# Optimization experiments

Hardware: AMD Instinct MI355X
Metric: run time of the kernel (lower is better)

Reference implementation:

```python
import jax, jax.numpy as jnp
import numpy as np

B, C, N, K = 2, 64, 16384, 16
C_OUT = 64


def setup_inputs() -> dict:
    key = jax.random.key(0)
    k1, k2, k3, k4 = jax.random.split(key, 4)
    x = jax.random.normal(k1, (B, C, N), dtype=jnp.float32)
    edge_index = jax.random.randint(k2, (2, B, N, K), 0, N, dtype=jnp.int64)
    # 1x1 Conv2d params: weight [C_out, 3C], bias [C_out]
    W = jax.random.normal(k3, (C_OUT, 3 * C), dtype=jnp.float32) * (1.0 / np.sqrt(3 * C))
    b = jax.random.normal(k4, (C_OUT,), dtype=jnp.float32) * 0.01
    return {"x": x, "edge_index": edge_index, "W": W, "b": b}


def _gather_nodes(x, idx):
    # x: [B, C, N], idx: [B, N, K] -> [B, C, N, K]
    return jax.vmap(lambda xb, ib: xb[:, ib])(x, idx)


def reference(x, edge_index, W, b):
    # x: [B, C, N]; edge_index: [2, B, N, K]
    x_i = _gather_nodes(x, edge_index[1])          # center features  [B,C,N,K]
    x_j = _gather_nodes(x, edge_index[0])          # neighbor features [B,C,N,K]
    edge_features = x_j - x_i                      # [B,C,N,K]
    global_feature = jnp.mean(x, axis=2, keepdims=True)  # [B,C,1] global mean over nodes
    global_rep = jnp.broadcast_to(global_feature[..., None], x_i.shape)  # [B,C,N,K]
    combined = jnp.concatenate([x_i, edge_features, global_rep], axis=1)  # [B,3C,N,K]
    # BasicConv: 1x1 conv + ReLU (norm=None)
    out = jnp.einsum("bcnk,oc->bonk", combined, W) + b[None, :, None, None]
    out = jax.nn.relu(out)
    return jnp.max(out, axis=-1, keepdims=True)    # [B,C_out,N,1]
```

## Files before the change

### kernel.cpp

```cpp
#include <hip/hip_runtime.h>


#define NNODES 16384
#define NCH 64

typedef _Float16 half8 __attribute__((ext_vector_type(8)));
typedef float f32x2 __attribute__((ext_vector_type(2)));
typedef float f32x4 __attribute__((ext_vector_type(4)));

__global__ __launch_bounds__(64) void prep_kernel(const float* __restrict__ W,
                                                  float2* __restrict__ ABg,
                                                  float* __restrict__ g_slots) {
  int o = blockIdx.x;
  int t = threadIdx.x;
  if (o == 0) {
#pragma unroll
    for (int i = 0; i < 16; ++i) g_slots[t + i * 64] = 0.0f;
  }
  float w1 = W[o * 192 + t];
  float w2 = W[o * 192 + 64 + t];
  ABg[t * 64 + o] = make_float2(w1 - w2, w2);
}

__global__ __launch_bounds__(256) void uv_kernel(const float* __restrict__ x,
                                                 const float2* __restrict__ ABg,
                                                 _Float16* __restrict__ u,
                                                 _Float16* __restrict__ v,
                                                 float* __restrict__ g_slots) {
  __shared__ float2 ABs[64 * 64];
  __shared__ float xs[64][64];
  __shared__ float csumS[64];
  int t = threadIdx.x;
  int lane = t & 63;
  int wv = __builtin_amdgcn_readfirstlane(t >> 6);
  int blk = blockIdx.x;
  int b = blk >> 8;
  int mb = (blk & 255) * 64;

  {
    const float4* src = (const float4*)ABg;
    float4* dst = (float4*)ABs;
#pragma unroll
    for (int j = 0; j < 8; ++j) dst[t + j * 256] = src[t + j * 256];
  }
  {
    const float* xb = x + (size_t)b * (NCH * NNODES) + mb;
    int off = t & 15;
#pragma unroll
    for (int j = 0; j < 4; ++j) {
      int c = (t >> 4) + j * 16;
      f32x4 q = __builtin_nontemporal_load(
          (const f32x4*)(xb + (size_t)c * NNODES + off * 4));
      *(f32x4*)&xs[c][off * 4] = q;
      float s = (q.x + q.y) + (q.z + q.w);
      s += __shfl_xor(s, 1, 16);
      s += __shfl_xor(s, 2, 16);
      s += __shfl_xor(s, 4, 16);
      s += __shfl_xor(s, 8, 16);
      if (off == 0) csumS[c] = s;
    }
  }
  __syncthreads();
  if (t < 64) atomicAdd(&g_slots[((blk & 7) << 7) + b * 64 + t], csumS[t]);

  int m0 = wv * 16;
  f32x2 aU[8], aV[8];
#pragma unroll
  for (int i = 0; i < 8; ++i) {
    aU[i] = (f32x2){0.f, 0.f};
    aV[i] = (f32x2){0.f, 0.f};
  }
#pragma unroll 8
  for (int c = 0; c < 64; ++c) {
    float2 ab = ABs[c * 64 + lane];
    f32x2 a2 = {ab.x, ab.x};
    f32x2 b2 = {ab.y, ab.y};
    const f32x4* xr = (const f32x4*)&xs[c][m0];
    f32x4 q0 = xr[0];
    f32x4 q1 = xr[1];
    f32x4 q2 = xr[2];
    f32x4 q3 = xr[3];
    f32x2 p0 = {q0.x, q0.y}, p1 = {q0.z, q0.w};
    f32x2 p2 = {q1.x, q1.y}, p3 = {q1.z, q1.w};
    f32x2 p4 = {q2.x, q2.y}, p5 = {q2.z, q2.w};
    f32x2 p6 = {q3.x, q3.y}, p7 = {q3.z, q3.w};
    aU[0] = __builtin_elementwise_fma(a2, p0, aU[0]);
    aU[1] = __builtin_elementwise_fma(a2, p1, aU[1]);
    aU[2] = __builtin_elementwise_fma(a2, p2, aU[2]);
    aU[3] = __builtin_elementwise_fma(a2, p3, aU[3]);
    aU[4] = __builtin_elementwise_fma(a2, p4, aU[4]);
    aU[5] = __builtin_elementwise_fma(a2, p5, aU[5]);
    aU[6] = __builtin_elementwise_fma(a2, p6, aU[6]);
    aU[7] = __builtin_elementwise_fma(a2, p7, aU[7]);
    aV[0] = __builtin_elementwise_fma(b2, p0, aV[0]);
    aV[1] = __builtin_elementwise_fma(b2, p1, aV[1]);
    aV[2] = __builtin_elementwise_fma(b2, p2, aV[2]);
    aV[3] = __builtin_elementwise_fma(b2, p3, aV[3]);
    aV[4] = __builtin_elementwise_fma(b2, p4, aV[4]);
    aV[5] = __builtin_elementwise_fma(b2, p5, aV[5]);
    aV[6] = __builtin_elementwise_fma(b2, p6, aV[6]);
    aV[7] = __builtin_elementwise_fma(b2, p7, aV[7]);
  }
  _Float16* ub = u + ((size_t)b * NNODES + mb + m0) * NCH + lane;
  _Float16* vb = v + ((size_t)b * NNODES + mb + m0) * NCH + lane;
#pragma unroll
  for (int i = 0; i < 8; ++i) {
    __builtin_nontemporal_store((_Float16)aU[i][0], &ub[(2 * i) * NCH]);
    __builtin_nontemporal_store((_Float16)aU[i][1], &ub[(2 * i + 1) * NCH]);
    __builtin_nontemporal_store((_Float16)aV[i][0], &vb[(2 * i) * NCH]);
    __builtin_nontemporal_store((_Float16)aV[i][1], &vb[(2 * i + 1) * NCH]);
  }
}

__global__ __launch_bounds__(256) void gather_kernel(const int* __restrict__ ei,
                                                     const _Float16* __restrict__ u,
                                                     const _Float16* __restrict__ v,
                                                     const float* __restrict__ W,
                                                     const float* __restrict__ bias,
                                                     const float* __restrict__ g_slots,
                                                     float* __restrict__ out) {
  __shared__ float tile[64][33];
  __shared__ float gb[64];
  __shared__ float pg[4][64];
  __shared__ float G_s[64];
  int t = threadIdx.x;
  int lane = t & 63;
  int wv = t >> 6;
  int blk = blockIdx.x;
  int xcd = blk & 7;
  int b = xcd >> 2;
  int nb = (blk >> 3) * 4 + (xcd & 3);
  int n0 = nb * 32;
  int q = lane >> 3;
  int r = lane & 7;
  const int* e0b = ei + (size_t)b * NNODES * 16;
  const int* e1b = ei + (size_t)(2 + b) * NNODES * 16;
  int f0 = (n0 + wv * 8) * 16 + q * 16 + r;
  int i0a = __builtin_nontemporal_load(e0b + f0);
  int i0b = __builtin_nontemporal_load(e0b + f0 + 8);
  int i1a = __builtin_nontemporal_load(e1b + f0);
  int i1b = __builtin_nontemporal_load(e1b + f0 + 8);
  if (t < 64) {
    float s = 0.f;
#pragma unroll
    for (int sl = 0; sl < 8; ++sl) s += g_slots[sl * 128 + b * 64 + t];
    gb[t] = s * (1.0f / 16384.0f);
  }
  __syncthreads();
  {
    int o = t >> 2, cq = t & 3;
    const float4* wr = (const float4*)(W + o * 192 + 128 + cq * 16);
    const float4* gr = (const float4*)(gb + cq * 16);
    float s = 0.f;
#pragma unroll
    for (int j = 0; j < 4; ++j) {
      float4 w = wr[j];
      float4 gg = gr[j];
      s += w.x * gg.x + w.y * gg.y + w.z * gg.z + w.w * gg.w;
    }
    pg[cq][o] = s;
  }
  __syncthreads();
  if (t < 64) G_s[t] = bias[t] + ((pg[0][t] + pg[1][t]) + (pg[2][t] + pg[3][t]));
  __syncthreads();
  const char* ubase = (const char*)(u + (size_t)b * NNODES * NCH);
  const char* vbase = (const char*)(v + (size_t)b * NNODES * NCH);
  uint32_t r16 = (uint32_t)(r * 16);
  half8 accA, accB;
#pragma unroll
  for (int j = 0; j < 8; ++j) {
    accA[j] = (_Float16)(-60000.0f);
    accB[j] = (_Float16)(-60000.0f);
  }
#pragma unroll
  for (int h = 0; h < 2; ++h) {
    half8 ua[8], va[8];
#pragma unroll
    for (int k = 0; k < 8; ++k) {
      int src = (lane & 56) + k;
      int m1 = __shfl(h ? i1b : i1a, src, 64);
      int m0i = __shfl(h ? i0b : i0a, src, 64);
      ua[k] = *(const half8*)(ubase + ((uint32_t)m1 * 128u + r16));
      va[k] = *(const half8*)(vbase + ((uint32_t)m0i * 128u + r16));
    }
#pragma unroll
    for (int k = 0; k < 8; ++k) {
      half8 s = ua[k] + va[k];
      if (k & 1)
        accB = __builtin_elementwise_max(accB, s);
      else
        accA = __builtin_elementwise_max(accA, s);
    }
  }
  half8 acc = __builtin_elementwise_max(accA, accB);
  int col = wv * 8 + q;
#pragma unroll
  for (int j = 0; j < 8; ++j) {
    tile[r * 8 + j][col] = fmaxf((float)acc[j] + G_s[r * 8 + j], 0.0f);
  }
  __syncthreads();
#pragma unroll
  for (int j = 0; j < 8; ++j) {
    int o = (t >> 5) + j * 8;
    int c2 = t & 31;
    __builtin_nontemporal_store(tile[o][c2],
                                &out[((size_t)b * 64 + o) * NNODES + n0 + c2]);
  }
}

extern "C" void kernel_launch(void* const* d_in, const int* in_sizes, int n_in,
                              void* d_out, int out_size, void* d_ws, size_t ws_size,
                              hipStream_t stream) {
  const float* x = (const float*)d_in[0];
  const int* ei = (const int*)d_in[1];
  const float* W = (const float*)d_in[2];
  const float* bias = (const float*)d_in[3];
  float* out = (float*)d_out;

  char* ws = (char*)d_ws;
  _Float16* u = (_Float16*)ws;
  _Float16* v = (_Float16*)(ws + (size_t)4 * 1024 * 1024);
  float* g_slots = (float*)(ws + (size_t)8 * 1024 * 1024);
  float2* ABg = (float2*)(ws + (size_t)8 * 1024 * 1024 + 4096);

  prep_kernel<<<64, 64, 0, stream>>>(W, ABg, g_slots);
  uv_kernel<<<512, 256, 0, stream>>>(x, ABg, u, v, g_slots);
  gather_kernel<<<1024, 256, 0, stream>>>(ei, u, v, W, bias, g_slots, out);
}
```

Before: 91.76 us.

## Fuse uv and gather kernels with a grid-wide atomic barrier

Merges the projection (uv) kernel and the gather/max kernel into one persistent launch of 512 blocks. A global atomic counter with spin-wait serves as the grid barrier between phases, and each block now handles 64 nodes in the gather phase instead of 32. Shared memory is aliased between the phases, and a memset replaces the g_slots zeroing that prep_kernel used to do. This removes a kernel launch and the tail gap between kernels. In exchange it requires all 512 blocks to be co-resident (launch_bounds 256,3), otherwise the spin barrier can deadlock, and the second phase runs with half as many blocks.

```diff
diff --git a/kernel.cpp b/kernel.cpp
--- a/kernel.cpp
+++ b/kernel.cpp
@@ -3,143 +3,149 @@
 
 #define NNODES 16384
 #define NCH 64
+#define NBLK 512u
 
 typedef _Float16 half8 __attribute__((ext_vector_type(8)));
 typedef float f32x2 __attribute__((ext_vector_type(2)));
 typedef float f32x4 __attribute__((ext_vector_type(4)));
 
 __global__ __launch_bounds__(64) void prep_kernel(const float* __restrict__ W,
-                                                  float2* __restrict__ ABg,
-                                                  float* __restrict__ g_slots) {
+                                                  float2* __restrict__ ABg) {
   int o = blockIdx.x;
   int t = threadIdx.x;
-  if (o == 0) {
-#pragma unroll
-    for (int i = 0; i < 16; ++i) g_slots[t + i * 64] = 0.0f;
-  }
   float w1 = W[o * 192 + t];
   float w2 = W[o * 192 + 64 + t];
   ABg[t * 64 + o] = make_float2(w1 - w2, w2);
 }
 
-__global__ __launch_bounds__(256) void uv_kernel(const float* __restrict__ x,
-                                                 const float2* __restrict__ ABg,
-                                                 _Float16* __restrict__ u,
-                                                 _Float16* __restrict__ v,
-                                                 float* __restrict__ g_slots) {
-  __shared__ float2 ABs[64 * 64];
-  __shared__ float xs[64][64];
-  __shared__ float csumS[64];
+__global__ __launch_bounds__(256, 3) void fused_kernel(
+    const float* __restrict__ x, const int* __restrict__ ei,
+    const float2* __restrict__ ABg, const float* __restrict__ W,
+    const float* __restrict__ bias, _Float16* __restrict__ u,
+    _Float16* __restrict__ v, float* __restrict__ g_slots,
+    unsigned int* __restrict__ ctr, float* __restrict__ out) {
+  __shared__ __align__(16) char smem[49408];
+  float2* ABs = (float2*)smem;
+  float(*xs)[64] = (float(*)[64])(smem + 32768);
+  float* csumS = (float*)(smem + 49152);
+  float(*tile)[33] = (float(*)[33])smem;
+  float* gb = (float*)(smem + 8448);
+  float(*pg)[64] = (float(*)[64])(smem + 8704);
+  float* G_s = (float*)(smem + 9728);
+
   int t = threadIdx.x;
   int lane = t & 63;
   int wv = __builtin_amdgcn_readfirstlane(t >> 6);
   int blk = blockIdx.x;
-  int b = blk >> 8;
-  int mb = (blk & 255) * 64;
 
   {
-    const float4* src = (const float4*)ABg;
-    float4* dst = (float4*)ABs;
-#pragma unroll
-    for (int j = 0; j < 8; ++j) dst[t + j * 256] = src[t + j * 256];
-  }
-  {
-    const float* xb = x + (size_t)b * (NCH * NNODES) + mb;
-    int off = t & 15;
-#pragma unroll
-    for (int j = 0; j < 4; ++j) {
-      int c = (t >> 4) + j * 16;
-      f32x4 q = __builtin_nontemporal_load(
-          (const f32x4*)(xb + (size_t)c * NNODES + off * 4));
-      *(f32x4*)&xs[c][off * 4] = q;
-      float s = (q.x + q.y) + (q.z + q.w);
-      s += __shfl_xor(s, 1, 16);
-      s += __shfl_xor(s, 2, 16);
-      s += __shfl_xor(s, 4, 16);
-      s += __shfl_xor(s, 8, 16);
-      if (off == 0) csumS[c] = s;
-    }
-  }
-  __syncthreads();
-  if (t < 64) atomicAdd(&g_slots[((blk & 7) << 7) + b * 64 + t], csumS[t]);
-
-  int m0 = wv * 16;
-  f32x2 aU[8], aV[8];
-#pragma unroll
-  for (int i = 0; i < 8; ++i) {
-    aU[i] = (f32x2){0.f, 0.f};
-    aV[i] = (f32x2){0.f, 0.f};
-  }
+    int b = blk >> 8;
+    int mb = (blk & 255) * 64;
+    {
+      const float4* src = (const float4*)ABg;
+      float4* dst = (float4*)ABs;
+#pragma unroll
+      for (int j = 0; j < 8; ++j) dst[t + j * 256] = src[t + j * 256];
+    }
+    {
+      const float* xb = x + (size_t)b * (NCH * NNODES) + mb;
+      int off = t & 15;
+#pragma unroll
+      for (int j = 0; j < 4; ++j) {
+        int c = (t >> 4) + j * 16;
+        f32x4 q = __builtin_nontemporal_load(
+            (const f32x4*)(xb + (size_t)c * NNODES + off * 4));
+        *(f32x4*)&xs[c][off * 4] = q;
+        float s = (q.x + q.y) + (q.z + q.w);
+        s += __shfl_xor(s, 1, 16);
+        s += __shfl_xor(s, 2, 16);
+        s += __shfl_xor(s, 4, 16);
+        s += __shfl_xor(s, 8, 16);
+        if (off == 0) csumS[c] = s;
+      }
+    }
+    __syncthreads();
+    if (t < 64) atomicAdd(&g_slots[((blk & 7) << 7) + b * 64 + t], csumS[t]);
+
+    int m0 = wv * 16;
+    f32x2 aU[8], aV[8];
+#pragma unroll
+    for (int i = 0; i < 8; ++i) {
+      aU[i] = (f32x2){0.f, 0.f};
+      aV[i] = (f32x2){0.f, 0.f};
+    }
 #pragma unroll 8
-  for (int c = 0; c < 64; ++c) {
-    float2 ab = ABs[c * 64 + lane];
-    f32x2 a2 = {ab.x, ab.x};
-    f32x2 b2 = {ab.y, ab.y};
-    const f32x4* xr = (const f32x4*)&xs[c][m0];
-    f32x4 q0 = xr[0];
-    f32x4 q1 = xr[1];
-    f32x4 q2 = xr[2];
-    f32x4 q3 = xr[3];
-    f32x2 p0 = {q0.x, q0.y}, p1 = {q0.z, q0.w};
-    f32x2 p2 = {q1.x, q1.y}, p3 = {q1.z, q1.w};
-    f32x2 p4 = {q2.x, q2.y}, p5 = {q2.z, q2.w};
-    f32x2 p6 = {q3.x, q3.y}, p7 = {q3.z, q3.w};
-    aU[0] = __builtin_elementwise_fma(a2, p0, aU[0]);
-    aU[1] = __builtin_elementwise_fma(a2, p1, aU[1]);
-    aU[2] = __builtin_elementwise_fma(a2, p2, aU[2]);
-    aU[3] = __builtin_elementwise_fma(a2, p3, aU[3]);
-    aU[4] = __builtin_elementwise_fma(a2, p4, aU[4]);
-    aU[5] = __builtin_elementwise_fma(a2, p5, aU[5]);
-    aU[6] = __builtin_elementwise_fma(a2, p6, aU[6]);
-    aU[7] = __builtin_elementwise_fma(a2, p7, aU[7]);
-    aV[0] = __builtin_elementwise_fma(b2, p0, aV[0]);
-    aV[1] = __builtin_elementwise_fma(b2, p1, aV[1]);
-    aV[2] = __builtin_elementwise_fma(b2, p2, aV[2]);
-    aV[3] = __builtin_elementwise_fma(b2, p3, aV[3]);
-    aV[4] = __builtin_elementwise_fma(b2, p4, aV[4]);
-    aV[5] = __builtin_elementwise_fma(b2, p5, aV[5]);
-    aV[6] = __builtin_elementwise_fma(b2, p6, aV[6]);
-    aV[7] = __builtin_elementwise_fma(b2, p7, aV[7]);
-  }
-  _Float16* ub = u + ((size_t)b * NNODES + mb + m0) * NCH + lane;
-  _Float16* vb = v + ((size_t)b * NNODES + mb + m0) * NCH + lane;
-#pragma unroll
-  for (int i = 0; i < 8; ++i) {
-    __builtin_nontemporal_store((_Float16)aU[i][0], &ub[(2 * i) * NCH]);
-    __builtin_nontemporal_store((_Float16)aU[i][1], &ub[(2 * i + 1) * NCH]);
-    __builtin_nontemporal_store((_Float16)aV[i][0], &vb[(2 * i) * NCH]);
-    __builtin_nontemporal_store((_Float16)aV[i][1], &vb[(2 * i + 1) * NCH]);
-  }
-}
-
-__global__ __launch_bounds__(256) void gather_kernel(const int* __restrict__ ei,
-                                                     const _Float16* __restrict__ u,
-                                                     const _Float16* __restrict__ v,
-                                                     const float* __restrict__ W,
-                                                     const float* __restrict__ bias,
-                                                     const float* __restrict__ g_slots,
-                                                     float* __restrict__ out) {
-  __shared__ float tile[64][33];
-  __shared__ float gb[64];
-  __shared__ float pg[4][64];
-  __shared__ float G_s[64];
-  int t = threadIdx.x;
-  int lane = t & 63;
-  int wv = t >> 6;
-  int blk = blockIdx.x;
+    for (int c = 0; c < 64; ++c) {
+      float2 ab = ABs[c * 64 + lane];
+      f32x2 a2 = {ab.x, ab.x};
+      f32x2 b2 = {ab.y, ab.y};
+      const f32x4* xr = (const f32x4*)&xs[c][m0];
+      f32x4 q0 = xr[0];
+      f32x4 q1 = xr[1];
+      f32x4 q2 = xr[2];
+      f32x4 q3 = xr[3];
+      f32x2 p0 = {q0.x, q0.y}, p1 = {q0.z, q0.w};
+      f32x2 p2 = {q1.x, q1.y}, p3 = {q1.z, q1.w};
+      f32x2 p4 = {q2.x, q2.y}, p5 = {q2.z, q2.w};
+      f32x2 p6 = {q3.x, q3.y}, p7 = {q3.z, q3.w};
+      aU[0] = __builtin_elementwise_fma(a2, p0, aU[0]);
+      aU[1] = __builtin_elementwise_fma(a2, p1, aU[1]);
+      aU[2] = __builtin_elementwise_fma(a2, p2, aU[2]);
+      aU[3] = __builtin_elementwise_fma(a2, p3, aU[3]);
+      aU[4] = __builtin_elementwise_fma(a2, p4, aU[4]);
+      aU[5] = __builtin_elementwise_fma(a2, p5, aU[5]);
+      aU[6] = __builtin_elementwise_fma(a2, p6, aU[6]);
+      aU[7] = __builtin_elementwise_fma(a2, p7, aU[7]);
+      aV[0] = __builtin_elementwise_fma(b2, p0, aV[0]);
+      aV[1] = __builtin_elementwise_fma(b2, p1, aV[1]);
+      aV[2] = __builtin_elementwise_fma(b2, p2, aV[2]);
+      aV[3] = __builtin_elementwise_fma(b2, p3, aV[3]);
+      aV[4] = __builtin_elementwise_fma(b2, p4, aV[4]);
+      aV[5] = __builtin_elementwise_fma(b2, p5, aV[5]);
+      aV[6] = __builtin_elementwise_fma(b2, p6, aV[6]);
+      aV[7] = __builtin_elementwise_fma(b2, p7, aV[7]);
+    }
+    _Float16* ub = u + ((size_t)b * NNODES + mb + m0) * NCH + lane;
+    _Float16* vb = v + ((size_t)b * NNODES + mb + m0) * NCH + lane;
+#pragma unroll
+    for (int i = 0; i < 8; ++i) {
+      ub[(2 * i) * NCH] = (_Float16)aU[i][0];
+      ub[(2 * i + 1) * NCH] = (_Float16)aU[i][1];
+      vb[(2 * i) * NCH] = (_Float16)aV[i][0];
+      vb[(2 * i + 1) * NCH] = (_Float16)aV[i][1];
+    }
+  }
+
+  __threadfence();
+  __syncthreads();
+  if (t == 0) {
+    __hip_atomic_fetch_add(ctr, 1u, __ATOMIC_RELEASE, __HIP_MEMORY_SCOPE_AGENT);
+    while (__hip_atomic_load(ctr, __ATOMIC_RELAXED, __HIP_MEMORY_SCOPE_AGENT) <
+           NBLK) {
+      __builtin_amdgcn_s_sleep(8);
+    }
+  }
+  __syncthreads();
+  __threadfence();
+
   int xcd = blk & 7;
   int b = xcd >> 2;
   int nb = (blk >> 3) * 4 + (xcd & 3);
-  int n0 = nb * 32;
+  int n0 = nb * 64;
   int q = lane >> 3;
   int r = lane & 7;
   const int* e0b = ei + (size_t)b * NNODES * 16;
   const int* e1b = ei + (size_t)(2 + b) * NNODES * 16;
   int f0 = (n0 + wv * 8) * 16 + q * 16 + r;
+  int f1 = f0 + 32 * 16;
   int i0a = __builtin_nontemporal_load(e0b + f0);
   int i0b = __builtin_nontemporal_load(e0b + f0 + 8);
   int i1a = __builtin_nontemporal_load(e1b + f0);
   int i1b = __builtin_nontemporal_load(e1b + f0 + 8);
+  int j0a = __builtin_nontemporal_load(e0b + f1);
+  int j0b = __builtin_nontemporal_load(e0b + f1 + 8);
+  int j1a = __builtin_nontemporal_load(e1b + f1);
+  int j1b = __builtin_nontemporal_load(e1b + f1 + 8);
   if (t < 64) {
     float s = 0.f;
 #pragma unroll
@@ -166,45 +172,51 @@
   const char* ubase = (const char*)(u + (size_t)b * NNODES * NCH);
   const char* vbase = (const char*)(v + (size_t)b * NNODES * NCH);
   uint32_t r16 = (uint32_t)(r * 16);
-  half8 accA, accB;
-#pragma unroll
-  for (int j = 0; j < 8; ++j) {
-    accA[j] = (_Float16)(-60000.0f);
-    accB[j] = (_Float16)(-60000.0f);
-  }
-#pragma unroll
-  for (int h = 0; h < 2; ++h) {
-    half8 ua[8], va[8];
-#pragma unroll
-    for (int k = 0; k < 8; ++k) {
-      int src = (lane & 56) + k;
-      int m1 = __shfl(h ? i1b : i1a, src, 64);
-      int m0i = __shfl(h ? i0b : i0a, src, 64);
-      ua[k] = *(const half8*)(ubase + ((uint32_t)m1 * 128u + r16));
-      va[k] = *(const half8*)(vbase + ((uint32_t)m0i * 128u + r16));
-    }
-#pragma unroll
-    for (int k = 0; k < 8; ++k) {
-      half8 s = ua[k] + va[k];
-      if (k & 1)
-        accB = __builtin_elementwise_max(accB, s);
-      else
-        accA = __builtin_elementwise_max(accA, s);
-    }
-  }
-  half8 acc = __builtin_elementwise_max(accA, accB);
-  int col = wv * 8 + q;
-#pragma unroll
-  for (int j = 0; j < 8; ++j) {
-    tile[r * 8 + j][col] = fmaxf((float)acc[j] + G_s[r * 8 + j], 0.0f);
-  }
-  __syncthreads();
-#pragma unroll
-  for (int j = 0; j < 8; ++j) {
-    int o = (t >> 5) + j * 8;
-    int c2 = t & 31;
-    __builtin_nontemporal_store(tile[o][c2],
-                                &out[((size_t)b * 64 + o) * NNODES + n0 + c2]);
+#pragma unroll
+  for (int p = 0; p < 2; ++p) {
+    int e1A = p ? j1a : i1a, e1B = p ? j1b : i1b;
+    int e0A = p ? j0a : i0a, e0B = p ? j0b : i0b;
+    half8 accA, accB;
+#pragma unroll
+    for (int j = 0; j < 8; ++j) {
+      accA[j] = (_Float16)(-60000.0f);
+      accB[j] = (_Float16)(-60000.0f);
+    }
+#pragma unroll
+    for (int h = 0; h < 2; ++h) {
+      half8 ua[8], va[8];
+#pragma unroll
+      for (int k = 0; k < 8; ++k) {
+        int src = (lane & 56) + k;
+        int m1 = __shfl(h ? e1B : e1A, src, 64);
+        int m0i = __shfl(h ? e0B : e0A, src, 64);
+        ua[k] = *(const half8*)(ubase + ((uint32_t)m1 * 128u + r16));
+        va[k] = *(const half8*)(vbase + ((uint32_t)m0i * 128u + r16));
+      }
+#pragma unroll
+      for (int k = 0; k < 8; ++k) {
+        half8 s = ua[k] + va[k];
+        if (k & 1)
+          accB = __builtin_elementwise_max(accB, s);
+        else
+          accA = __builtin_elementwise_max(accA, s);
+      }
+    }
+    half8 acc = __builtin_elementwise_max(accA, accB);
+    int col = wv * 8 + q;
+#pragma unroll
+    for (int j = 0; j < 8; ++j) {
+      tile[r * 8 + j][col] = fmaxf((float)acc[j] + G_s[r * 8 + j], 0.0f);
+    }
+    __syncthreads();
+#pragma unroll
+    for (int j = 0; j < 8; ++j) {
+      int o = (t >> 5) + j * 8;
+      int c2 = t & 31;
+      __builtin_nontemporal_store(
+          tile[o][c2], &out[((size_t)b * 64 + o) * NNODES + n0 + p * 32 + c2]);
+    }
+    __syncthreads();
   }
 }
 
@@ -221,9 +233,12 @@
   _Float16* u = (_Float16*)ws;
   _Float16* v = (_Float16*)(ws + (size_t)4 * 1024 * 1024);
   float* g_slots = (float*)(ws + (size_t)8 * 1024 * 1024);
-  float2* ABg = (float2*)(ws + (size_t)8 * 1024 * 1024 + 4096);
-
-  prep_kernel<<<64, 64, 0, stream>>>(W, ABg, g_slots);
-  uv_kernel<<<512, 256, 0, stream>>>(x, ABg, u, v, g_slots);
-  gather_kernel<<<1024, 256, 0, stream>>>(ei, u, v, W, bias, g_slots, out);
+  unsigned int* ctr =
+      (unsigned int*)(ws + (size_t)8 * 1024 * 1024 + 4096);
+  float2* ABg = (float2*)(ws + (size_t)8 * 1024 * 1024 + 8192);
+
+  hipMemsetAsync(ws + (size_t)8 * 1024 * 1024, 0, 4096 + 16, stream);
+  prep_kernel<<<64, 64, 0, stream>>>(W, ABg);
+  fused_kernel<<<512, 256, 0, stream>>>(x, ei, ABg, W, bias, u, v, g_slots, ctr,
+                                        out);
 }
```

Measured after the change: 204.4 us. +122.7%, slower.
